# Kernel optimization log

Measured on AMD Instinct MI355X. Metric: run time of the kernel, lower is better.

Reference implementation:

```python
import jax, jax.numpy as jnp
import numpy as np
from jax import lax

B, T, HID, H, DK, DV, K = 2, 2048, 1024, 16, 64, 64, 4
SCALE = float(DK) ** -0.5
EPS = 1e-5


def setup_inputs() -> dict:
    key = jax.random.key(0)
    ks = jax.random.split(key, 12)
    n = lambda k, sh, s=0.02: (jax.random.normal(k, sh, jnp.float32) * s)
    return {
        "x": jax.random.normal(ks[0], (B, T, HID), jnp.float32),
        "Wq": n(ks[1], (H * DK, HID)),
        "Wk": n(ks[2], (H * DK, HID)),
        "Wv": n(ks[3], (H * DV, HID)),
        "Wa": n(ks[4], (H * DV, HID)), "ba": jnp.zeros((H * DV,), jnp.float32),
        "Wb": n(ks[5], (H, HID)), "bb": jnp.zeros((H,), jnp.float32),
        "Wg": n(ks[6], (H * DV, HID)),
        "Wo": n(ks[7], (HID, H * DV)),
        "qcw": n(ks[8], (H * DK, 1, K), 0.3), "qcb": jnp.zeros((H * DK,), jnp.float32),
        "kcw": n(ks[9], (H * DK, 1, K), 0.3), "kcb": jnp.zeros((H * DK,), jnp.float32),
        "vcw": n(ks[10], (H * DV, 1, K), 0.3), "vcb": jnp.zeros((H * DV,), jnp.float32),
        "ln_w": jnp.ones((DV,), jnp.float32), "ln_b": jnp.zeros((DV,), jnp.float32),
    }


def _causal_dwconv_silu(z, w, b):
    # z: [B,T,C], w: [C,1,K] depthwise. Conv1d(padding=K-1) then slice[:T] == causal left-pad.
    zc = z.transpose(0, 2, 1)  # [B,C,T]
    y = lax.conv_general_dilated(zc, w, (1,), [(K - 1, 0)],
                                 dimension_numbers=("NCH", "OIH", "NCH"),
                                 feature_group_count=zc.shape[1])
    return jax.nn.silu((y + b[None, :, None]).transpose(0, 2, 1))


def reference(x, Wq, Wk, Wv, Wa, ba, Wb, bb, Wg, Wo,
              qcw, qcb, kcw, kcb, vcw, vcb, ln_w, ln_b):
    Bb, Tt, _ = x.shape
    q = _causal_dwconv_silu(x @ Wq.T, qcw, qcb).reshape(Bb, Tt, H, DK)
    k = _causal_dwconv_silu(x @ Wk.T, kcw, kcb).reshape(Bb, Tt, H, DK) * SCALE
    v = _causal_dwconv_silu(x @ Wv.T, vcw, vcb).reshape(Bb, Tt, H, DV)
    a = jax.nn.sigmoid(x @ Wa.T + ba).reshape(Bb, Tt, H, DV)
    beta = jax.nn.sigmoid(x @ Wb.T + bb)  # [B,T,H]

    def step(S, inp):
        qt, kt, vt, at, bt = inp  # qt/kt: [B,H,DK], vt/at: [B,H,DV], bt: [B,H]
        err = jnp.einsum("bhij,bhj->bhi", S, kt) - vt          # S@k - v
        S = at[..., None] * S - bt[..., None, None] * (err[..., None] * kt[:, :, None, :])
        o = jnp.einsum("bhij,bhj->bhi", S, qt)                 # S@q
        return S, o

    xs = tuple(jnp.moveaxis(t, 1, 0) for t in (q, k, v, a, beta))  # time-leading
    S0 = jnp.zeros((Bb, H, DV, DK), x.dtype)
    _, o = lax.scan(step, S0, xs)
    o = jnp.moveaxis(o, 0, 1)  # [B,T,H,DV]

    mu = o.mean(-1, keepdims=True)
    var = ((o - mu) ** 2).mean(-1, keepdims=True)
    o = (o - mu) / jnp.sqrt(var + EPS) * ln_w + ln_b

    g = jax.nn.sigmoid(x @ Wg.T).reshape(Bb, Tt, H, DV)
    o = (o * g).reshape(Bb, Tt, H * DV)
    return o @ Wo.T
```

## Files before the change

### kernel.cpp

```cpp
#include <hip/hip_runtime.h>
#include <hip/hip_bf16.h>
#include <cstdint>


using bf16 = __hip_bfloat16;
typedef __bf16 bf16x8 __attribute__((ext_vector_type(8)));
typedef __bf16 bf16x4v __attribute__((ext_vector_type(4)));
typedef float f32x4 __attribute__((ext_vector_type(4)));
typedef float f32x2 __attribute__((ext_vector_type(2)));
typedef unsigned int u32x4 __attribute__((ext_vector_type(4)));
typedef unsigned int u32x2 __attribute__((ext_vector_type(2)));

__device__ __forceinline__ __bf16 cvt_bf16(float f) {
  __hip_bfloat16 h = (__hip_bfloat16)f;
  return *reinterpret_cast<__bf16*>(&h);
}
__device__ __forceinline__ void async_copy16(const void* g, void* l) {
  __builtin_amdgcn_global_load_lds((const __attribute__((address_space(1))) void*)g,
                                   (__attribute__((address_space(3))) void*)l,
                                   16, 0, 0);
}
__device__ __forceinline__ float bcf(unsigned int u) { return __builtin_bit_cast(float, u); }
template <int CTRL>
__device__ __forceinline__ float dpp_f(float x) {
  int y = __builtin_amdgcn_update_dpp(0, __builtin_bit_cast(int, x), CTRL, 0xF, 0xF, true);
  return __builtin_bit_cast(float, y);
}

__global__ __launch_bounds__(256) void cvtw_kernel(
    const float* __restrict__ x, const float* __restrict__ Wq,
    const float* __restrict__ Wk, const float* __restrict__ Wv,
    const float* __restrict__ Wa, const float* __restrict__ Wg,
    const float* __restrict__ Wo, bf16* __restrict__ xb,
    bf16* __restrict__ w4b, bf16* __restrict__ wgb, bf16* __restrict__ wob)
{
  int blk = blockIdx.x;
  const float* src;
  __bf16* dst;
  size_t off;
  if (blk < 4096) {
    src = x; dst = (__bf16*)xb;
    off = (size_t)blk * 1024 + threadIdx.x * 4;
  } else if (blk < 8192) {
    int wb = blk - 4096;
    int wi = wb >> 10;
    src = (wi == 0) ? Wq : (wi == 1) ? Wk : (wi == 2) ? Wv : Wa;
    dst = (__bf16*)w4b + (size_t)wi * 1024 * 1024;
    off = (size_t)(wb & 1023) * 1024 + threadIdx.x * 4;
  } else if (blk < 9216) {
    src = Wg; dst = (__bf16*)wgb;
    off = (size_t)(blk - 8192) * 1024 + threadIdx.x * 4;
  } else {
    src = Wo; dst = (__bf16*)wob;
    off = (size_t)(blk - 9216) * 1024 + threadIdx.x * 4;
  }
  float4 f = *(const float4*)(src + off);
  bf16x4v t;
  t[0] = cvt_bf16(f.x); t[1] = cvt_bf16(f.y); t[2] = cvt_bf16(f.z); t[3] = cvt_bf16(f.w);
  *(bf16x4v*)(dst + off) = t;
}

template <int MODE, bool A_FP32>
__global__ __launch_bounds__(256) void gemm_bt(
    const void* __restrict__ Av, const float* __restrict__ Bt,
    const float* __restrict__ bias, float* __restrict__ Cf, bf16* __restrict__ Cb,
    int M, int N, int K)
{
  __shared__ __align__(16) __bf16 As[128 * 32];
  __shared__ __align__(16) __bf16 Bs[128 * 32];

  const int tid  = threadIdx.x;
  const int lane = tid & 63;
  const int wave = tid >> 6;
  const int tile_m = blockIdx.y * 128;
  const int tile_n = blockIdx.x * 128;
  const int wm = (wave >> 1) * 64;
  const int wn = (wave & 1) * 64;

  const int srow = lane >> 2;
  const int scol = (lane & 3) * 8;

  f32x4 acc[4][4];
#pragma unroll
  for (int i = 0; i < 4; ++i)
#pragma unroll
    for (int j = 0; j < 4; ++j) acc[i][j] = {0.f, 0.f, 0.f, 0.f};

  for (int k0 = 0; k0 < K; k0 += 32) {
    float4 b0[2], b1[2], a0[2], a1[2];
#pragma unroll
    for (int s = 0; s < 2; ++s) {
      int brow = tile_n + s * 64 + wave * 16 + srow;
      if (brow > N - 1) brow = N - 1;
      const float* bp = Bt + (size_t)brow * K + k0 + scol;
      b0[s] = *(const float4*)bp;
      b1[s] = *(const float4*)(bp + 4);
      if (A_FP32) {
        int arow = tile_m + s * 64 + wave * 16 + srow;
        const float* ap = (const float*)Av + (size_t)arow * K + k0 + scol;
        a0[s] = *(const float4*)ap;
        a1[s] = *(const float4*)(ap + 4);
      }
    }
    __syncthreads();
#pragma unroll
    for (int s = 0; s < 2; ++s) {
      if (!A_FP32) {
        int arow = tile_m + s * 64 + wave * 16 + srow;
        async_copy16((const __bf16*)Av + (size_t)arow * K + k0 + scol,
                     &As[(s * 64 + wave * 16 + srow) * 32 + scol]);
      } else {
        bf16x8 ua;
        ua[0] = cvt_bf16(a0[s].x); ua[1] = cvt_bf16(a0[s].y);
        ua[2] = cvt_bf16(a0[s].z); ua[3] = cvt_bf16(a0[s].w);
        ua[4] = cvt_bf16(a1[s].x); ua[5] = cvt_bf16(a1[s].y);
        ua[6] = cvt_bf16(a1[s].z); ua[7] = cvt_bf16(a1[s].w);
        *(bf16x8*)&As[(s * 64 + wave * 16 + srow) * 32 + scol] = ua;
      }
      bf16x8 u;
      u[0] = cvt_bf16(b0[s].x); u[1] = cvt_bf16(b0[s].y);
      u[2] = cvt_bf16(b0[s].z); u[3] = cvt_bf16(b0[s].w);
      u[4] = cvt_bf16(b1[s].x); u[5] = cvt_bf16(b1[s].y);
      u[6] = cvt_bf16(b1[s].z); u[7] = cvt_bf16(b1[s].w);
      *(bf16x8*)&Bs[(s * 64 + wave * 16 + srow) * 32 + scol] = u;
    }
    __syncthreads();

    bf16x8 af[4], bfr[4];
#pragma unroll
    for (int i = 0; i < 4; ++i)
      af[i] = *(const bf16x8*)&As[(wm + i * 16 + (lane & 15)) * 32 + (lane >> 4) * 8];
#pragma unroll
    for (int j = 0; j < 4; ++j)
      bfr[j] = *(const bf16x8*)&Bs[(wn + j * 16 + (lane & 15)) * 32 + (lane >> 4) * 8];

#pragma unroll
    for (int i = 0; i < 4; ++i)
#pragma unroll
      for (int j = 0; j < 4; ++j)
        acc[i][j] = __builtin_amdgcn_mfma_f32_16x16x32_bf16(af[i], bfr[j], acc[i][j], 0, 0, 0);
  }

#pragma unroll
  for (int i = 0; i < 4; ++i) {
#pragma unroll
    for (int j = 0; j < 4; ++j) {
#pragma unroll
      for (int r = 0; r < 4; ++r) {
        int gm = tile_m + wm + i * 16 + (lane >> 4) * 4 + r;
        int gn = tile_n + wn + j * 16 + (lane & 15);
        if (gn < N) {
          float val = acc[i][j][r];
          if (MODE == 3 || MODE == 5) {
            float bv = bias ? bias[gn] : 0.f;
            val = 1.f / (1.f + __expf(-(val + bv)));
          }
          if (MODE == 4)      Cf[(size_t)gm * N + gn] = val;
          else if (MODE == 5) Cf[(size_t)gn * M + gm] = val;
          else                Cb[(size_t)gm * N + gn] = (bf16)val;
        }
      }
    }
  }
}

__global__ __launch_bounds__(256) void gemm_bb_ln(
    const bf16* __restrict__ o, const bf16* __restrict__ g,
    const float* __restrict__ lnw, const float* __restrict__ lnb,
    const bf16* __restrict__ Bw, float* __restrict__ C)
{
  __shared__ __align__(16) __bf16 As2[128][72];
  __shared__ __align__(16) __bf16 Bs[128 * 32];
  __shared__ float sW[64], sB[64];

  const int tid  = threadIdx.x;
  const int lane = tid & 63;
  const int wave = tid >> 6;
  const int tile_m = blockIdx.y * 128;
  const int tile_n = blockIdx.x * 128;
  const int wm = (wave >> 1) * 64;
  const int wn = (wave & 1) * 64;
  const int srow = lane >> 2;
  const int scol = (lane & 3) * 8;
  const int rl = tid >> 1;
  const int half = tid & 1;

  if (tid < 64) { sW[tid] = lnw[tid]; sB[tid] = lnb[tid]; }

  f32x4 acc[4][4];
#pragma unroll
  for (int i = 0; i < 4; ++i)
#pragma unroll
    for (int j = 0; j < 4; ++j) acc[i][j] = {0.f, 0.f, 0.f, 0.f};

  for (int h = 0; h < 16; ++h) {
    __syncthreads();

    const __bf16* op = (const __bf16*)o + (size_t)(tile_m + rl) * 1024 + h * 64 + half * 32;
    const __bf16* gp = (const __bf16*)g + (size_t)(tile_m + rl) * 1024 + h * 64 + half * 32;
    bf16x8 ov0 = *(const bf16x8*)(op);
    bf16x8 ov1 = *(const bf16x8*)(op + 8);
    bf16x8 ov2 = *(const bf16x8*)(op + 16);
    bf16x8 ov3 = *(const bf16x8*)(op + 24);
    bf16x8 gv0 = *(const bf16x8*)(gp);
    bf16x8 gv1 = *(const bf16x8*)(gp + 8);
    bf16x8 gv2 = *(const bf16x8*)(gp + 16);
    bf16x8 gv3 = *(const bf16x8*)(gp + 24);

    float sum = 0.f;
#pragma unroll
    for (int e = 0; e < 8; ++e)
      sum += (float)ov0[e] + (float)ov1[e] + (float)ov2[e] + (float)ov3[e];
    sum += __shfl_xor(sum, 1);
    float mu = sum * (1.f / 64.f);
    float vv = 0.f;
#pragma unroll
    for (int e = 0; e < 8; ++e) {
      float d0 = (float)ov0[e] - mu, d1 = (float)ov1[e] - mu;
      float d2 = (float)ov2[e] - mu, d3 = (float)ov3[e] - mu;
      vv += d0 * d0 + d1 * d1 + d2 * d2 + d3 * d3;
    }
    vv += __shfl_xor(vv, 1);
    float rstd = rsqrtf(vv * (1.f / 64.f) + 1e-5f);

    bf16x8 res0, res1, res2, res3;
#pragma unroll
    for (int e = 0; e < 8; ++e) {
      int c0 = half * 32 + e;
      res0[e] = cvt_bf16((((float)ov0[e] - mu) * rstd * sW[c0] + sB[c0]) * (float)gv0[e]);
      res1[e] = cvt_bf16((((float)ov1[e] - mu) * rstd * sW[c0 + 8] + sB[c0 + 8]) * (float)gv1[e]);
      res2[e] = cvt_bf16((((float)ov2[e] - mu) * rstd * sW[c0 + 16] + sB[c0 + 16]) * (float)gv2[e]);
      res3[e] = cvt_bf16((((float)ov3[e] - mu) * rstd * sW[c0 + 24] + sB[c0 + 24]) * (float)gv3[e]);
    }
    *(bf16x8*)&As2[rl][half * 32 + 0]  = res0;
    *(bf16x8*)&As2[rl][half * 32 + 8]  = res1;
    *(bf16x8*)&As2[rl][half * 32 + 16] = res2;
    *(bf16x8*)&As2[rl][half * 32 + 24] = res3;

#pragma unroll
    for (int sub = 0; sub < 2; ++sub) {
      if (sub) __syncthreads();
      int k0 = h * 64 + sub * 32;
#pragma unroll
      for (int s = 0; s < 2; ++s) {
        int brow = tile_n + s * 64 + wave * 16 + srow;
        async_copy16((const __bf16*)Bw + (size_t)brow * 1024 + k0 + scol,
                     &Bs[(s * 64 + wave * 16 + srow) * 32 + scol]);
      }
      __syncthreads();

      bf16x8 af[4], bfr[4];
#pragma unroll
      for (int i = 0; i < 4; ++i)
        af[i] = *(const bf16x8*)&As2[wm + i * 16 + (lane & 15)][(lane >> 4) * 8 + sub * 32];
#pragma unroll
      for (int j = 0; j < 4; ++j)
        bfr[j] = *(const bf16x8*)&Bs[(wn + j * 16 + (lane & 15)) * 32 + (lane >> 4) * 8];

#pragma unroll
      for (int i = 0; i < 4; ++i)
#pragma unroll
        for (int j = 0; j < 4; ++j)
          acc[i][j] = __builtin_amdgcn_mfma_f32_16x16x32_bf16(af[i], bfr[j], acc[i][j], 0, 0, 0);
    }
  }

#pragma unroll
  for (int i = 0; i < 4; ++i)
#pragma unroll
    for (int j = 0; j < 4; ++j)
#pragma unroll
      for (int r = 0; r < 4; ++r) {
        int gm = tile_m + wm + i * 16 + (lane >> 4) * 4 + r;
        int gn = tile_n + wn + j * 16 + (lane & 15);
        C[(size_t)gm * 1024 + gn] = acc[i][j][r];
      }
}

__global__ __launch_bounds__(256) void mega_gemm2(
    const bf16* __restrict__ Av, const bf16* __restrict__ W4b,
    const float* __restrict__ Wb, const float* __restrict__ bb,
    const float* __restrict__ ba, bf16* __restrict__ C4,
    float* __restrict__ betab)
{
  __shared__ __align__(16) __bf16 As[128 * 32];
  __shared__ __align__(16) __bf16 Bs[128 * 32];

  const int tid  = threadIdx.x;
  const int lane = tid & 63;
  const int wave = tid >> 6;
  const int tile_m = blockIdx.y * 128;
  const bool isbeta = (blockIdx.x >= 32);
  const int tile_n = isbeta ? 0 : blockIdx.x * 128;
  const int grp = tile_n >> 10;
  const int tnl = tile_n & 1023;
  const int wm = (wave >> 1) * 64;
  const int wn = (wave & 1) * 64;

  const int srow = lane >> 2;
  const int scol = (lane & 3) * 8;

  f32x4 acc[4][4];
#pragma unroll
  for (int i = 0; i < 4; ++i)
#pragma unroll
    for (int j = 0; j < 4; ++j) acc[i][j] = {0.f, 0.f, 0.f, 0.f};

  const __bf16* Wp = (const __bf16*)W4b + (size_t)grp * 1024 * 1024;

  for (int k0 = 0; k0 < 1024; k0 += 32) {
    float4 b0[2], b1[2];
    if (isbeta) {
#pragma unroll
      for (int s = 0; s < 2; ++s) {
        int brow = s * 64 + wave * 16 + srow;
        if (brow > 15) brow = 15;
        const float* bp = Wb + (size_t)brow * 1024 + k0 + scol;
        b0[s] = *(const float4*)bp;
        b1[s] = *(const float4*)(bp + 4);
      }
    }
    __syncthreads();
#pragma unroll
    for (int s = 0; s < 2; ++s) {
      int arow = tile_m + s * 64 + wave * 16 + srow;
      async_copy16((const __bf16*)Av + (size_t)arow * 1024 + k0 + scol,
                   &As[(s * 64 + wave * 16 + srow) * 32 + scol]);
      if (!isbeta) {
        int brow = tnl + s * 64 + wave * 16 + srow;
        async_copy16(Wp + (size_t)brow * 1024 + k0 + scol,
                     &Bs[(s * 64 + wave * 16 + srow) * 32 + scol]);
      } else {
        bf16x8 u;
        u[0] = cvt_bf16(b0[s].x); u[1] = cvt_bf16(b0[s].y);
        u[2] = cvt_bf16(b0[s].z); u[3] = cvt_bf16(b0[s].w);
        u[4] = cvt_bf16(b1[s].x); u[5] = cvt_bf16(b1[s].y);
        u[6] = cvt_bf16(b1[s].z); u[7] = cvt_bf16(b1[s].w);
        *(bf16x8*)&Bs[(s * 64 + wave * 16 + srow) * 32 + scol] = u;
      }
    }
    __syncthreads();

    bf16x8 af[4], bfr[4];
#pragma unroll
    for (int i = 0; i < 4; ++i)
      af[i] = *(const bf16x8*)&As[(wm + i * 16 + (lane & 15)) * 32 + (lane >> 4) * 8];
#pragma unroll
    for (int j = 0; j < 4; ++j)
      bfr[j] = *(const bf16x8*)&Bs[(wn + j * 16 + (lane & 15)) * 32 + (lane >> 4) * 8];

#pragma unroll
    for (int i = 0; i < 4; ++i)
#pragma unroll
      for (int j = 0; j < 4; ++j)
        acc[i][j] = __builtin_amdgcn_mfma_f32_16x16x32_bf16(af[i], bfr[j], acc[i][j], 0, 0, 0);
  }

  if (!isbeta) {
    bf16* Cp = (bf16*)((__bf16*)C4 + (size_t)grp * 4096 * 1024);
#pragma unroll
    for (int i = 0; i < 4; ++i)
#pragma unroll
      for (int j = 0; j < 4; ++j)
#pragma unroll
        for (int r = 0; r < 4; ++r) {
          int gm = tile_m + wm + i * 16 + (lane >> 4) * 4 + r;
          int col = tnl + wn + j * 16 + (lane & 15);
          float val = acc[i][j][r];
          if (grp == 3) val = 1.f / (1.f + __expf(-(val + ba[col])));
          ((__bf16*)Cp)[(size_t)gm * 1024 + col] = cvt_bf16(val);
        }
  } else {
#pragma unroll
    for (int i = 0; i < 4; ++i)
#pragma unroll
      for (int j = 0; j < 4; ++j)
#pragma unroll
        for (int r = 0; r < 4; ++r) {
          int gm = tile_m + wm + i * 16 + (lane >> 4) * 4 + r;
          int gn = wn + j * 16 + (lane & 15);
          if (gn < 16) {
            float val = 1.f / (1.f + __expf(-(acc[i][j][r] + bb[gn])));
            betab[(size_t)gn * 4096 + gm] = val;
          }
        }
  }
}

__device__ __forceinline__ void conv_body(
    int idx, const bf16* __restrict__ z, const float* __restrict__ w,
    const float* __restrict__ bias, bf16* __restrict__ out, float scale)
{
  int c8 = idx & 127;
  int m  = idx >> 7;
  int t  = m & 2047;
  int c0 = c8 * 8;

  const __bf16* base = (const __bf16*)z + (size_t)m * 1024 + c0;
  const bf16x8 zzero = __builtin_bit_cast(bf16x8, (u32x4){0u, 0u, 0u, 0u});
  bf16x8 z3 = *(const bf16x8*)base;
  bf16x8 z2 = (t >= 1) ? *(const bf16x8*)(base - 1024) : zzero;
  bf16x8 z1 = (t >= 2) ? *(const bf16x8*)(base - 2048) : zzero;
  bf16x8 z0 = (t >= 3) ? *(const bf16x8*)(base - 3072) : zzero;

  const float* wp = w + c0 * 4;
  bf16x8 res;
#pragma unroll
  for (int e = 0; e < 8; ++e) {
    float4 we = *(const float4*)(wp + e * 4);
    float acc = bias[c0 + e] + (float)z3[e] * we.w;
    acc += (float)z2[e] * we.z;
    acc += (float)z1[e] * we.y;
    acc += (float)z0[e] * we.x;
    float s = acc / (1.f + __expf(-acc));
    res[e] = cvt_bf16(s * scale);
  }
  *(bf16x8*)((__bf16*)out + (size_t)m * 1024 + c0) = res;
}

__global__ __launch_bounds__(256) void conv_silu_kernel(
    const bf16* __restrict__ z, const float* __restrict__ w,
    const float* __restrict__ bias, bf16* __restrict__ out, float scale)
{
  conv_body(blockIdx.x * 256 + threadIdx.x, z, w, bias, out, scale);
}

__global__ __launch_bounds__(256) void conv2_kernel(
    const bf16* __restrict__ zq, const bf16* __restrict__ zk,
    const float* __restrict__ qcw, const float* __restrict__ qcb,
    const float* __restrict__ kcw, const float* __restrict__ kcb,
    bf16* __restrict__ oq, bf16* __restrict__ ok)
{
  int sec = blockIdx.x >> 11;
  int bx  = blockIdx.x & 2047;
  int idx = bx * 256 + threadIdx.x;
  if (sec == 0) conv_body(idx, zq, qcw, qcb, oq, 1.f);
  else          conv_body(idx, zk, kcw, kcb, ok, 0.125f);
}

__global__ __launch_bounds__(256) void convv_kk_kernel(
    const bf16* __restrict__ zv, const float* __restrict__ vcw,
    const float* __restrict__ vcb, bf16* __restrict__ ov,
    const bf16* __restrict__ k, const float* __restrict__ betab,
    float* __restrict__ G)
{
  if (blockIdx.x < 2048) {
    conv_body(blockIdx.x * 256 + threadIdx.x, zv, vcw, vcb, ov, 1.f);
    return;
  }
  int gtid = (blockIdx.x - 2048) * 256 + threadIdx.x;
  int out = gtid >> 2;
  int j   = gtid & 3;
  int h = out >> 12;
  int m = out & 4095;
  int t = m & 2047;
  float s = 0.f;
  if (t > 0) {
    const __bf16* r1 = (const __bf16*)k + (size_t)m * 1024 + h * 64 + j * 16;
    const __bf16* r0 = r1 - 1024;
    bf16x8 a0 = *(const bf16x8*)r0;
    bf16x8 a1 = *(const bf16x8*)(r0 + 8);
    bf16x8 b0 = *(const bf16x8*)r1;
    bf16x8 b1 = *(const bf16x8*)(r1 + 8);
#pragma unroll
    for (int e = 0; e < 8; ++e)
      s += (float)a0[e] * (float)b0[e] + (float)a1[e] * (float)b1[e];
  }
  s += __shfl_xor(s, 1);
  s += __shfl_xor(s, 2);
  if (j == 0) G[out] = betab[out] * s;
}

__global__ __launch_bounds__(256) void kk_kernel(
    const bf16* __restrict__ k, const float* __restrict__ betab,
    float* __restrict__ G)
{
  int tid = blockIdx.x * 256 + threadIdx.x;
  int out = tid >> 2;
  int j   = tid & 3;
  int h = out >> 12;
  int m = out & 4095;
  int t = m & 2047;
  float s = 0.f;
  if (t > 0) {
    const __bf16* r1 = (const __bf16*)k + (size_t)m * 1024 + h * 64 + j * 16;
    const __bf16* r0 = r1 - 1024;
    bf16x8 a0 = *(const bf16x8*)r0;
    bf16x8 a1 = *(const bf16x8*)(r0 + 8);
    bf16x8 b0 = *(const bf16x8*)r1;
    bf16x8 b1 = *(const bf16x8*)(r1 + 8);
#pragma unroll
    for (int e = 0; e < 8; ++e)
      s += (float)a0[e] * (float)b0[e] + (float)a1[e] * (float)b1[e];
  }
  s += __shfl_xor(s, 1);
  s += __shfl_xor(s, 2);
  if (j == 0) G[out] = betab[out] * s;
}

#define SCAN_STEP(i, KN0, KN1, Q0, Q1, WV, WA, BT, GT, LAST)                  \
  {                                                                           \
    const float vr = ((i) & 1) ? bcf((WV) & 0xffff0000u) : bcf((WV) << 16);   \
    const float ar = ((i) & 1) ? bcf((WA) & 0xffff0000u) : bcf((WA) << 16);   \
    float unxt = 0.f;                                                         \
    f32x2 k2n0 = {0.f, 0.f}, k2n1 = {0.f, 0.f};                               \
    if (!(LAST)) {                                                            \
      k2n0 = unpk(KN0); k2n1 = unpk(KN1);                                     \
      f32x2 dd = S20 * k2n0; dd += S21 * k2n1;                                \
      unxt = dd[0] + dd[1];                                                   \
      unxt += dpp_f<0xB1>(unxt);  unxt += dpp_f<0x4E>(unxt);                  \
      unxt += dpp_f<0x141>(unxt); unxt += dpp_f<0x140>(unxt);                 \
    } else { Sold0 = S20; Sold1 = S21; }                                      \
    float A_ = (BT) * __builtin_fmaf(aprev, u, -vr);                          \
    cc = __builtin_fmaf(-cc, (GT), A_);                                       \
    f32x2 q20 = unpk(Q0), q21 = unpk(Q1);                                     \
    const f32x2 cc2 = {cc, cc}, arv = {ar, ar};                               \
    f32x2 oo;                                                                 \
    { f32x2 t0 = cc2 * k2c0; S20 = arv * S20 - t0; oo = S20 * q20;            \
      f32x2 t1 = cc2 * k2c1; S21 = arv * S21 - t1; oo += S21 * q21; }         \
    so[(i)][lane] = oo[0] + oo[1];                                            \
    aprev = ar;                                                               \
    if (!(LAST)) { k2c0 = k2n0; k2c1 = k2n1; u = unxt; }                      \
  }

#define LOADG(KS, QS, VS, AS, BS, GS, g)                                      \
  KS = *(const u32x4*)&skT[buf][sg][(g) * 8];                                 \
  QS = *(const u32x4*)&sqT[buf][sg][(g) * 8];                                 \
  VS = *(const unsigned int*)&svaT[buf][0][r4][(g) * 2];                      \
  AS = *(const unsigned int*)&svaT[buf][1][r4][(g) * 2];                      \
  BS = *(const f32x2*)&sbeta[c * 16 + (g) * 2];                               \
  GS = *(const f32x2*)&sG[c * 16 + (g) * 2];

__global__ __launch_bounds__(256) void scan_gemm_kernel(
    const bf16* __restrict__ q, const bf16* __restrict__ k,
    const bf16* __restrict__ v, const bf16* __restrict__ a,
    const float* __restrict__ betab, const float* __restrict__ gkk,
    bf16* __restrict__ o,
    const float* __restrict__ x, const bf16* __restrict__ Wgb,
    bf16* __restrict__ gout)
{
  __shared__ __align__(16) __bf16 skT[2][16][72];
  __shared__ __align__(16) __bf16 sqT[2][16][72];
  __shared__ __align__(16) __bf16 svaT[2][2][4][16];
  __shared__ __align__(16) float  so[16][68];
  __shared__ __align__(16) __bf16 so2[16][4];
  __shared__ float sbeta[2048];
  __shared__ float sG[2048];
  __shared__ __align__(16) __bf16 As[128 * 32];
  __shared__ __align__(16) __bf16 Bs[128 * 32];

  if (blockIdx.x >= 512) {
    const int gb   = blockIdx.x - 512;
    const int tid  = threadIdx.x;
    const int lane = tid & 63;
    const int wave = tid >> 6;
    const int tile_m = (gb >> 3) * 128;
    const int tile_n = (gb & 7) * 128;
    const int wm = (wave >> 1) * 64;
    const int wn = (wave & 1) * 64;
    const int srow = lane >> 2;
    const int scol = (lane & 3) * 8;

    f32x4 acc[4][4];
#pragma unroll
    for (int i = 0; i < 4; ++i)
#pragma unroll
      for (int j = 0; j < 4; ++j) acc[i][j] = {0.f, 0.f, 0.f, 0.f};

    for (int k0 = 0; k0 < 1024; k0 += 32) {
      float4 a0[2], a1[2];
#pragma unroll
      for (int s = 0; s < 2; ++s) {
        int arow = tile_m + s * 64 + wave * 16 + srow;
        const float* ap = x + (size_t)arow * 1024 + k0 + scol;
        a0[s] = *(const float4*)ap;
        a1[s] = *(const float4*)(ap + 4);
      }
      __syncthreads();
#pragma unroll
      for (int s = 0; s < 2; ++s) {
        bf16x8 ua;
        ua[0] = cvt_bf16(a0[s].x); ua[1] = cvt_bf16(a0[s].y);
        ua[2] = cvt_bf16(a0[s].z); ua[3] = cvt_bf16(a0[s].w);
        ua[4] = cvt_bf16(a1[s].x); ua[5] = cvt_bf16(a1[s].y);
        ua[6] = cvt_bf16(a1[s].z); ua[7] = cvt_bf16(a1[s].w);
        *(bf16x8*)&As[(s * 64 + wave * 16 + srow) * 32 + scol] = ua;
        int brow = tile_n + s * 64 + wave * 16 + srow;
        async_copy16((const __bf16*)Wgb + (size_t)brow * 1024 + k0 + scol,
                     &Bs[(s * 64 + wave * 16 + srow) * 32 + scol]);
      }
      __syncthreads();

      bf16x8 af[4], bfr[4];
#pragma unroll
      for (int i = 0; i < 4; ++i)
        af[i] = *(const bf16x8*)&As[(wm + i * 16 + (lane & 15)) * 32 + (lane >> 4) * 8];
#pragma unroll
      for (int j = 0; j < 4; ++j)
        bfr[j] = *(const bf16x8*)&Bs[(wn + j * 16 + (lane & 15)) * 32 + (lane >> 4) * 8];

#pragma unroll
      for (int i = 0; i < 4; ++i)
#pragma unroll
        for (int j = 0; j < 4; ++j)
          acc[i][j] = __builtin_amdgcn_mfma_f32_16x16x32_bf16(af[i], bfr[j], acc[i][j], 0, 0, 0);
    }

#pragma unroll
    for (int i = 0; i < 4; ++i)
#pragma unroll
      for (int j = 0; j < 4; ++j)
#pragma unroll
        for (int r = 0; r < 4; ++r) {
          int gm = tile_m + wm + i * 16 + (lane >> 4) * 4 + r;
          int gn = tile_n + wn + j * 16 + (lane & 15);
          float val = 1.f / (1.f + __expf(-acc[i][j][r]));
          gout[(size_t)gm * 1024 + gn] = (bf16)val;
        }
    return;
  }

  if (threadIdx.x >= 64) return;

  const int blk = blockIdx.x;
  const int qd = blk >> 5;
  const int bh = blk & 31;
  const int b = bh >> 4, h = bh & 15;
  const int lane = threadIdx.x;
  const int r4 = lane >> 4;
  const int sg = lane & 15;

  {
    const float* bp = betab + (size_t)h * 4096 + b * 2048;
    const float* gp = gkk   + (size_t)h * 4096 + b * 2048;
    for (int t = lane; t < 2048; t += 64) { sbeta[t] = bp[t]; sG[t] = gp[t]; }
  }

  const size_t bkq = (size_t)b * 2048 * 1024 + h * 64;
  const size_t bva = bkq + qd * 4;
  const __bf16* kp = (const __bf16*)k;
  const __bf16* qp = (const __bf16*)q;

  const int g_st = lane >> 3;
  const int g_cg = (lane & 7) * 8;
  const int sgp  = (lane & 7) * 2;
  const int va_vh = (lane >> 4) & 1;
  const int va_st = lane & 15;

  bf16x8 pk0, pk1, pq0, pq1;
  bf16x4v pva;
  auto fetch = [&](int t0) {
    int st0 = t0 + g_st, st1 = t0 + 8 + g_st;
    pk0 = *(const bf16x8*)(kp + bkq + (size_t)st0 * 1024 + g_cg);
    pk1 = *(const bf16x8*)(kp + bkq + (size_t)st1 * 1024 + g_cg);
    pq0 = *(const bf16x8*)(qp + bkq + (size_t)st0 * 1024 + g_cg);
    pq1 = *(const bf16x8*)(qp + bkq + (size_t)st1 * 1024 + g_cg);
    if (lane < 32) {
      const __bf16* src = va_vh ? (const __bf16*)a : (const __bf16*)v;
      pva = *(const bf16x4v*)(src + bva + (size_t)(t0 + va_st) * 1024);
    }
  };
  auto commit = [&](int cb) {
    {
      u32x4 wk = __builtin_bit_cast(u32x4, pk0);
      u32x4 wq = __builtin_bit_cast(u32x4, pq0);
      u32x2 lo, hi;
      lo[0] = wk[0]; lo[1] = wk[1]; hi[0] = wk[2]; hi[1] = wk[3];
      *(u32x2*)&skT[cb][sgp][g_st * 4]     = lo;
      *(u32x2*)&skT[cb][sgp + 1][g_st * 4] = hi;
      lo[0] = wq[0]; lo[1] = wq[1]; hi[0] = wq[2]; hi[1] = wq[3];
      *(u32x2*)&sqT[cb][sgp][g_st * 4]     = lo;
      *(u32x2*)&sqT[cb][sgp + 1][g_st * 4] = hi;
    }
    {
      u32x4 wk = __builtin_bit_cast(u32x4, pk1);
      u32x4 wq = __builtin_bit_cast(u32x4, pq1);
      u32x2 lo, hi;
      lo[0] = wk[0]; lo[1] = wk[1]; hi[0] = wk[2]; hi[1] = wk[3];
      *(u32x2*)&skT[cb][sgp][(8 + g_st) * 4]     = lo;
      *(u32x2*)&skT[cb][sgp + 1][(8 + g_st) * 4] = hi;
      lo[0] = wq[0]; lo[1] = wq[1]; hi[0] = wq[2]; hi[1] = wq[3];
      *(u32x2*)&sqT[cb][sgp][(8 + g_st) * 4]     = lo;
      *(u32x2*)&sqT[cb][sgp + 1][(8 + g_st) * 4] = hi;
    }
    if (lane < 32) {
#pragma unroll
      for (int r = 0; r < 4; ++r) svaT[cb][va_vh][r][va_st] = pva[r];
    }
  };

  fetch(0); commit(0);

  f32x2 S20 = {0.f, 0.f}, S21 = {0.f, 0.f};
  f32x2 Sold0 = {0.f, 0.f}, Sold1 = {0.f, 0.f};
  float u = 0.f, cc = 0.f, aprev = 0.f;

  auto unpk = [&](unsigned int w) -> f32x2 {
    f32x2 r; r[0] = bcf(w << 16); r[1] = bcf(w & 0xffff0000u); return r;
  };

  for (int c = 0; c < 128; ++c) {
    const int buf = c & 1;
    const bool hasNext = (c + 1 < 128);

    if (hasNext) fetch((c + 1) * 16);

    u32x4 kA, qA, kB, qB, kC, qC;
    unsigned int vA, aA, vB, aB, vC, aC;
    f32x2 bA, gA, bB, gB, bC, gC;

    LOADG(kA, qA, vA, aA, bA, gA, 0)
    LOADG(kB, qB, vB, aB, bB, gB, 1)
    LOADG(kC, qC, vC, aC, bC, gC, 2)

    f32x2 k2c0 = unpk(kA[0]);
    f32x2 k2c1 = unpk(kA[1]);
    {
      f32x2 dd = Sold0 * k2c0;
      dd += Sold1 * k2c1;
      float un = dd[0] + dd[1];
      un += dpp_f<0xB1>(un);
      un += dpp_f<0x4E>(un);
      un += dpp_f<0x141>(un);
      un += dpp_f<0x140>(un);
      u = un;
    }

    SCAN_STEP(0,  kA[2], kA[3], qA[0], qA[1], vA, aA, bA[0], gA[0], false)
    SCAN_STEP(1,  kB[0], kB[1], qA[2], qA[3], vA, aA, bA[1], gA[1], false)
    LOADG(kA, qA, vA, aA, bA, gA, 3)
    SCAN_STEP(2,  kB[2], kB[3], qB[0], qB[1], vB, aB, bB[0], gB[0], false)
    SCAN_STEP(3,  kC[0], kC[1], qB[2], qB[3], vB, aB, bB[1], gB[1], false)
    LOADG(kB, qB, vB, aB, bB, gB, 4)
    SCAN_STEP(4,  kC[2], kC[3], qC[0], qC[1], vC, aC, bC[0], gC[0], false)
    SCAN_STEP(5,  kA[0], kA[1], qC[2], qC[3], vC, aC, bC[1], gC[1], false)
    LOADG(kC, qC, vC, aC, bC, gC, 5)
    SCAN_STEP(6,  kA[2], kA[3], qA[0], qA[1], vA, aA, bA[0], gA[0], false)
    SCAN_STEP(7,  kB[0], kB[1], qA[2], qA[3], vA, aA, bA[1], gA[1], false)
    LOADG(kA, qA, vA, aA, bA, gA, 6)
    SCAN_STEP(8,  kB[2], kB[3], qB[0], qB[1], vB, aB, bB[0], gB[0], false)
    SCAN_STEP(9,  kC[0], kC[1], qB[2], qB[3], vB, aB, bB[1], gB[1], false)
    LOADG(kB, qB, vB, aB, bB, gB, 7)
    SCAN_STEP(10, kC[2], kC[3], qC[0], qC[1], vC, aC, bC[0], gC[0], false)
    SCAN_STEP(11, kA[0], kA[1], qC[2], qC[3], vC, aC, bC[1], gC[1], false)
    SCAN_STEP(12, kA[2], kA[3], qA[0], qA[1], vA, aA, bA[0], gA[0], false)
    SCAN_STEP(13, kB[0], kB[1], qA[2], qA[3], vA, aA, bA[1], gA[1], false)
    SCAN_STEP(14, kB[2], kB[3], qB[0], qB[1], vB, aB, bB[0], gB[0], false)
    SCAN_STEP(15, kB[2], kB[3], qB[2], qB[3], vB, aB, bB[1], gB[1], true)

    {
      int st = lane >> 2, rr = lane & 3;
      float4 A0 = *(const float4*)&so[st][rr * 16];
      float4 A1 = *(const float4*)&so[st][rr * 16 + 4];
      float4 A2 = *(const float4*)&so[st][rr * 16 + 8];
      float4 A3 = *(const float4*)&so[st][rr * 16 + 12];
      float s = (((A0.x + A0.y) + (A0.z + A0.w)) + ((A1.x + A1.y) + (A1.z + A1.w)))
              + (((A2.x + A2.y) + (A2.z + A2.w)) + ((A3.x + A3.y) + (A3.z + A3.w)));
      so2[st][rr] = cvt_bf16(s);
    }
    if (lane < 16)
      *(bf16x4v*)((__bf16*)o + bva + (size_t)(c * 16 + lane) * 1024) =
          *(const bf16x4v*)&so2[lane][0];

    if (hasNext) commit(buf ^ 1);
  }
}

__global__ __launch_bounds__(256) void ln_gate_kernel(
    const bf16* __restrict__ o, const bf16* __restrict__ g,
    const float* __restrict__ lnw, const float* __restrict__ lnb,
    bf16* __restrict__ out)
{
  int row = blockIdx.x * 4 + (threadIdx.x >> 6);
  int lane = threadIdx.x & 63;
  size_t idx = (size_t)row * 64 + lane;
  float xv = (float)o[idx];
  float mu = xv;
#pragma unroll
  for (int s = 1; s < 64; s <<= 1) mu += __shfl_xor(mu, s);
  mu *= (1.f / 64.f);
  float d = xv - mu;
  float vv = d * d;
#pragma unroll
  for (int s = 1; s < 64; s <<= 1) vv += __shfl_xor(vv, s);
  vv *= (1.f / 64.f);
  float y = d * rsqrtf(vv + 1e-5f) * lnw[lane] + lnb[lane];
  y *= (float)g[idx];
  out[idx] = (bf16)y;
}

extern "C" void kernel_launch(void* const* d_in, const int* in_sizes, int n_in,
                              void* d_out, int out_size, void* d_ws, size_t ws_size,
                              hipStream_t stream)
{
  const float* x   = (const float*)d_in[0];
  const float* Wq  = (const float*)d_in[1];
  const float* Wk  = (const float*)d_in[2];
  const float* Wv  = (const float*)d_in[3];
  const float* Wa  = (const float*)d_in[4];
  const float* ba  = (const float*)d_in[5];
  const float* Wb  = (const float*)d_in[6];
  const float* bb  = (const float*)d_in[7];
  const float* Wg  = (const float*)d_in[8];
  const float* Wo  = (const float*)d_in[9];
  const float* qcw = (const float*)d_in[10];
  const float* qcb = (const float*)d_in[11];
  const float* kcw = (const float*)d_in[12];
  const float* kcb = (const float*)d_in[13];
  const float* vcw = (const float*)d_in[14];
  const float* vcb = (const float*)d_in[15];
  const float* lnw = (const float*)d_in[16];
  const float* lnb = (const float*)d_in[17];

  const int M = 4096, HID = 1024;
  const size_t PLANE = (size_t)M * HID;
  const size_t PB = PLANE * sizeof(bf16);

  char* ws = (char*)d_ws;
  float* outf = (float*)d_out;
  const bool rich = (ws_size >= 5 * PB + 1024);

  dim3 blk(256);
  dim3 g8(8, 32);
  int nconv = (int)((size_t)M * 128 / 256);

  if (rich) {
    bf16* P0 = (bf16*)(ws);
    bf16* P1 = (bf16*)(ws + PB);
    bf16* P2 = (bf16*)(ws + 2 * PB);
    bf16* P3 = (bf16*)(ws + 3 * PB);
    bf16* P4 = (bf16*)(ws + 4 * PB);
    bf16*  xb    = (bf16*)d_out;
    bf16*  W4b   = (bf16*)((char*)d_out + 8 * 1024 * 1024);
    bf16*  Kb    = xb;
    bf16*  Qb    = W4b;
    float* betab = (float*)P4;
    float* gkk   = (float*)((char*)P4 + 256 * 1024);
    bf16*  Wgb   = (bf16*)((char*)P4 + 1024 * 1024);
    bf16*  Wob   = (bf16*)((char*)P4 + 3 * 1024 * 1024);

    cvtw_kernel<<<10240, blk, 0, stream>>>(x, Wq, Wk, Wv, Wa, Wg, Wo,
                                           xb, W4b, Wgb, Wob);
    mega_gemm2<<<dim3(33, 32), blk, 0, stream>>>(xb, W4b, Wb, bb, ba, P0, betab);
    conv2_kernel<<<4096, blk, 0, stream>>>(P0, P1, qcw, qcb, kcw, kcb, Qb, Kb);
    convv_kk_kernel<<<3072, blk, 0, stream>>>(P2, vcw, vcb, P1, Kb, betab, gkk);
    scan_gemm_kernel<<<768, blk, 0, stream>>>(Qb, Kb, P1, P3, betab, gkk, P0,
                                              x, Wgb, P2);
    gemm_bb_ln<<<g8, blk, 0, stream>>>(P0, P2, lnw, lnb, Wob, outf);
  } else {
    bf16* P  = (bf16*)(ws);
    bf16* qb = (bf16*)(ws + PB);
    bf16* kb = (bf16*)(ws + 2 * PB);
    bf16* vb = (bf16*)(ws + 3 * PB);
    float* betab = (float*)d_out;
    float* gkk   = (float*)((char*)d_out + 256 * 1024);
    bf16*  ob    = (bf16*)((char*)d_out + 8 * 1024 * 1024);

    gemm_bt<2, true><<<g8, blk, 0, stream>>>(x, Wq, nullptr, nullptr, P, M, HID, HID);
    conv_silu_kernel<<<nconv, blk, 0, stream>>>(P, qcw, qcb, qb, 1.f);
    gemm_bt<2, true><<<g8, blk, 0, stream>>>(x, Wk, nullptr, nullptr, P, M, HID, HID);
    conv_silu_kernel<<<nconv, blk, 0, stream>>>(P, kcw, kcb, kb, 0.125f);
    gemm_bt<2, true><<<g8, blk, 0, stream>>>(x, Wv, nullptr, nullptr, P, M, HID, HID);
    conv_silu_kernel<<<nconv, blk, 0, stream>>>(P, vcw, vcb, vb, 1.f);
    gemm_bt<3, true><<<g8, blk, 0, stream>>>(x, Wa, ba, nullptr, P, M, HID, HID);
    gemm_bt<5, true><<<dim3(1, 32), blk, 0, stream>>>(x, Wb, bb, betab, nullptr, M, 16, HID);
    kk_kernel<<<1024, blk, 0, stream>>>(kb, betab, gkk);
    scan_gemm_kernel<<<512, blk, 0, stream>>>(qb, kb, vb, P, betab, gkk, ob,
                                              x, nullptr, nullptr);
    gemm_bt<3, true><<<g8, blk, 0, stream>>>(x, Wg, nullptr, nullptr, qb, M, HID, HID);
    ln_gate_kernel<<<M * 16 / 4, blk, 0, stream>>>(ob, qb, lnw, lnb, kb);
    gemm_bt<4, false><<<g8, blk, 0, stream>>>(kb, Wo, nullptr, outf, nullptr, M, HID, HID);
  }
}
```

Baseline: 457.4 us.

## Swizzle GEMM block order for XCD locality and prefetch LN inputs

Both GEMM kernels move to a 1D grid with a swizzled block index, so consecutive blocks on the same XCD (bx&7) share row tiles and weight tiles in L2. gemm_bb_ln now prefetches the next head's o/g vectors in registers before the barrier, overlapping global loads with the LayerNorm and MFMA work. The scan path raises wave priority and loads beta/gkk with float4 vectors. The prefetch adds register pressure, and the swizzle assumes 8 XCDs and fixed grid sizes.

After: 439.0 us. -4.0%, faster.

```diff
diff --git a/kernel.cpp b/kernel.cpp
--- a/kernel.cpp
+++ b/kernel.cpp
@@ -173,11 +173,14 @@
   __shared__ __align__(16) __bf16 Bs[128 * 32];
   __shared__ float sW[64], sB[64];
 
+  const int bx = blockIdx.x;
+  const int logical = (bx & 7) * 32 + (bx >> 3);
+  const int tile_m = (logical >> 3) * 128;
+  const int tile_n = (logical & 7) * 128;
+
   const int tid  = threadIdx.x;
   const int lane = tid & 63;
   const int wave = tid >> 6;
-  const int tile_m = blockIdx.y * 128;
-  const int tile_n = blockIdx.x * 128;
   const int wm = (wave >> 1) * 64;
   const int wn = (wave & 1) * 64;
   const int srow = lane >> 2;
@@ -187,25 +190,37 @@
 
   if (tid < 64) { sW[tid] = lnw[tid]; sB[tid] = lnb[tid]; }
 
+  const __bf16* obase = (const __bf16*)o + (size_t)(tile_m + rl) * 1024 + half * 32;
+  const __bf16* gbase = (const __bf16*)g + (size_t)(tile_m + rl) * 1024 + half * 32;
+
   f32x4 acc[4][4];
 #pragma unroll
   for (int i = 0; i < 4; ++i)
 #pragma unroll
     for (int j = 0; j < 4; ++j) acc[i][j] = {0.f, 0.f, 0.f, 0.f};
 
+  bf16x8 ov0, ov1, ov2, ov3, gv0, gv1, gv2, gv3;
+  {
+    const __bf16* op = obase;
+    const __bf16* gp = gbase;
+    ov0 = *(const bf16x8*)(op);      ov1 = *(const bf16x8*)(op + 8);
+    ov2 = *(const bf16x8*)(op + 16); ov3 = *(const bf16x8*)(op + 24);
+    gv0 = *(const bf16x8*)(gp);      gv1 = *(const bf16x8*)(gp + 8);
+    gv2 = *(const bf16x8*)(gp + 16); gv3 = *(const bf16x8*)(gp + 24);
+  }
+
   for (int h = 0; h < 16; ++h) {
+    bf16x8 nо0, nо1, nо2, nо3, ng0, ng1, ng2, ng3;
+    if (h + 1 < 16) {
+      const __bf16* op = obase + (h + 1) * 64;
+      const __bf16* gp = gbase + (h + 1) * 64;
+      nо0 = *(const bf16x8*)(op);      nо1 = *(const bf16x8*)(op + 8);
+      nо2 = *(const bf16x8*)(op + 16); nо3 = *(const bf16x8*)(op + 24);
+      ng0 = *(const bf16x8*)(gp);      ng1 = *(const bf16x8*)(gp + 8);
+      ng2 = *(const bf16x8*)(gp + 16); ng3 = *(const bf16x8*)(gp + 24);
+    }
+
     __syncthreads();
-
-    const __bf16* op = (const __bf16*)o + (size_t)(tile_m + rl) * 1024 + h * 64 + half * 32;
-    const __bf16* gp = (const __bf16*)g + (size_t)(tile_m + rl) * 1024 + h * 64 + half * 32;
-    bf16x8 ov0 = *(const bf16x8*)(op);
-    bf16x8 ov1 = *(const bf16x8*)(op + 8);
-    bf16x8 ov2 = *(const bf16x8*)(op + 16);
-    bf16x8 ov3 = *(const bf16x8*)(op + 24);
-    bf16x8 gv0 = *(const bf16x8*)(gp);
-    bf16x8 gv1 = *(const bf16x8*)(gp + 8);
-    bf16x8 gv2 = *(const bf16x8*)(gp + 16);
-    bf16x8 gv3 = *(const bf16x8*)(gp + 24);
 
     float sum = 0.f;
 #pragma unroll
@@ -263,6 +278,11 @@
         for (int j = 0; j < 4; ++j)
           acc[i][j] = __builtin_amdgcn_mfma_f32_16x16x32_bf16(af[i], bfr[j], acc[i][j], 0, 0, 0);
     }
+
+    if (h + 1 < 16) {
+      ov0 = nо0; ov1 = nо1; ov2 = nо2; ov3 = nо3;
+      gv0 = ng0; gv1 = ng1; gv2 = ng2; gv3 = ng3;
+    }
   }
 
 #pragma unroll
@@ -286,14 +306,23 @@
   __shared__ __align__(16) __bf16 As[128 * 32];
   __shared__ __align__(16) __bf16 Bs[128 * 32];
 
+  const int bx = blockIdx.x;
+  const bool isbeta = (bx >= 1024);
+  int tile_m, tile_n;
+  if (!isbeta) {
+    const int logical = (bx & 7) * 128 + (bx >> 3);
+    tile_m = (logical >> 5) * 128;
+    tile_n = (logical & 31) * 128;
+  } else {
+    tile_m = (bx - 1024) * 128;
+    tile_n = 0;
+  }
+  const int grp = tile_n >> 10;
+  const int tnl = tile_n & 1023;
+
   const int tid  = threadIdx.x;
   const int lane = tid & 63;
   const int wave = tid >> 6;
-  const int tile_m = blockIdx.y * 128;
-  const bool isbeta = (blockIdx.x >= 32);
-  const int tile_n = isbeta ? 0 : blockIdx.x * 128;
-  const int grp = tile_n >> 10;
-  const int tnl = tile_n & 1023;
   const int wm = (wave >> 1) * 64;
   const int wn = (wave & 1) * 64;
 
@@ -621,6 +650,7 @@
   }
 
   if (threadIdx.x >= 64) return;
+  __builtin_amdgcn_s_setprio(1);
 
   const int blk = blockIdx.x;
   const int qd = blk >> 5;
@@ -633,7 +663,10 @@
   {
     const float* bp = betab + (size_t)h * 4096 + b * 2048;
     const float* gp = gkk   + (size_t)h * 4096 + b * 2048;
-    for (int t = lane; t < 2048; t += 64) { sbeta[t] = bp[t]; sG[t] = gp[t]; }
+    for (int t4 = lane * 4; t4 < 2048; t4 += 256) {
+      *(float4*)&sbeta[t4] = *(const float4*)(bp + t4);
+      *(float4*)&sG[t4]    = *(const float4*)(gp + t4);
+    }
   }
 
   const size_t bkq = (size_t)b * 2048 * 1024 + h * 64;
@@ -841,12 +874,12 @@
 
     cvtw_kernel<<<10240, blk, 0, stream>>>(x, Wq, Wk, Wv, Wa, Wg, Wo,
                                            xb, W4b, Wgb, Wob);
-    mega_gemm2<<<dim3(33, 32), blk, 0, stream>>>(xb, W4b, Wb, bb, ba, P0, betab);
+    mega_gemm2<<<1056, blk, 0, stream>>>(xb, W4b, Wb, bb, ba, P0, betab);
     conv2_kernel<<<4096, blk, 0, stream>>>(P0, P1, qcw, qcb, kcw, kcb, Qb, Kb);
     convv_kk_kernel<<<3072, blk, 0, stream>>>(P2, vcw, vcb, P1, Kb, betab, gkk);
     scan_gemm_kernel<<<768, blk, 0, stream>>>(Qb, Kb, P1, P3, betab, gkk, P0,
                                               x, Wgb, P2);
-    gemm_bb_ln<<<g8, blk, 0, stream>>>(P0, P2, lnw, lnb, Wob, outf);
+    gemm_bb_ln<<<256, blk, 0, stream>>>(P0, P2, lnw, lnb, Wob, outf);
   } else {
     bf16* P  = (bf16*)(ws);
     bf16* qb = (bf16*)(ws + PB);
```
